# Performance work log

Measured on AMD Instinct MI355X. Metric: run time of the kernel, lower is better.

Reference implementation:

```python
import jax, jax.numpy as jnp
import numpy as np

B, S, EMB = 8, 1024, 512
H, DK = 8, 64
D_MODEL = 512


def setup_inputs() -> dict:
    key = jax.random.key(0)
    ks = jax.random.split(key, 12)
    s = 0.02
    return {
        "queries": jax.random.normal(ks[0], (B, S, EMB), jnp.float32),
        "keys": jax.random.normal(ks[1], (B, S, EMB), jnp.float32),
        "values": jax.random.normal(ks[2], (B, S, EMB), jnp.float32),
        "edges_key": jax.random.normal(ks[3], (S, S, DK), jnp.float32),
        "edges_value": jax.random.normal(ks[4], (S, S, DK), jnp.float32),
        "attn_bias": jax.random.normal(ks[5], (B, 1, S, S), jnp.float32),
        "Wq": jax.random.normal(ks[6], (EMB, H * DK), jnp.float32) * s,
        "bq": jnp.zeros((H * DK,), jnp.float32),
        "Wk": jax.random.normal(ks[7], (EMB, H * DK), jnp.float32) * s,
        "bk": jnp.zeros((H * DK,), jnp.float32),
        "Wv": jax.random.normal(ks[8], (EMB, H * DK), jnp.float32) * s,
        "bv": jnp.zeros((H * DK,), jnp.float32),
        "Wp": jax.random.normal(ks[9], (EMB, D_MODEL), jnp.float32) * s,
        "bp": jnp.zeros((D_MODEL,), jnp.float32),
    }


def _split_heads(x):
    b, s, _ = x.shape
    return x.reshape(b, s, H, DK).transpose(0, 2, 1, 3)  # [B,H,S,DK]


def reference(queries, keys, values, edges_key, edges_value, attn_bias,
              Wq, bq, Wk, bk, Wv, bv, Wp, bp):
    q = _split_heads(queries @ Wq + bq)
    k = _split_heads(keys @ Wk + bk)
    v = _split_heads(values @ Wv + bv)

    scaled_q = q * (DK ** -0.5)
    # standard scores + per-pair edge-key bias
    product = jnp.einsum('bhqd,bhkd->bhqk', scaled_q, k)
    edge_bias_k = jnp.einsum('bhqd,qkd->bhqk', scaled_q, edges_key)
    product = product + edge_bias_k + attn_bias

    weights = jax.nn.softmax(product, axis=-1)
    out = jnp.einsum('bhqk,bhkd->bhqd', weights, v)
    out = out + jnp.einsum('bhqk,qkd->bhqd', weights, edges_value)

    # combine heads: [B,H,S,DK] -> [B,S,H*DK]
    out = out.transpose(0, 2, 1, 3).reshape(queries.shape[0], queries.shape[1], H * DK)
    return out @ Wp + bp
```

## Files before the change

### kernel.cpp

```cpp
#include <hip/hip_runtime.h>
#include <cstdint>
#include <cstddef>


typedef __bf16 bf16x8 __attribute__((ext_vector_type(8)));
typedef float f32x4 __attribute__((ext_vector_type(4)));
typedef unsigned short u16x8 __attribute__((ext_vector_type(8)));
typedef unsigned short u16;

__device__ __forceinline__ u16 f2bf(float f) {
  unsigned int u = __float_as_uint(f);
  return (u16)((u + 0x7fffu + ((u >> 16) & 1u)) >> 16);
}

__device__ __forceinline__ float bf2f(u16 u) {
  return __uint_as_float(((unsigned int)u) << 16);
}

__device__ __forceinline__ bf16x8 ld8(const u16* p) {
  return __builtin_bit_cast(bf16x8, *(const u16x8*)p);
}

__device__ __forceinline__ bf16x8 cvt8(const float* p) {
  const float4 f1 = *(const float4*)p;
  const float4 f2 = *(const float4*)(p + 4);
  u16x8 u;
  u[0]=f2bf(f1.x); u[1]=f2bf(f1.y); u[2]=f2bf(f1.z); u[3]=f2bf(f1.w);
  u[4]=f2bf(f2.x); u[5]=f2bf(f2.y); u[6]=f2bf(f2.z); u[7]=f2bf(f2.w);
  return __builtin_bit_cast(bf16x8, u);
}

__device__ __forceinline__ f32x4 mfma16(bf16x8 a, bf16x8 b, f32x4 c) {
  return __builtin_amdgcn_mfma_f32_16x16x32_bf16(a, b, c, 0, 0, 0);
}

__global__ __launch_bounds__(256) void k0_weights(
    const float* __restrict__ Wq, const float* __restrict__ Wk,
    const float* __restrict__ Wv, const float* __restrict__ Wp,
    u16* __restrict__ WT) {
  const int idx = blockIdx.x * 256 + threadIdx.x;
  const int w = idx >> 18;
  const int rem = idx & 262143;
  const int o = rem >> 9, i = rem & 511;
  const float* W = (w == 0) ? Wq : (w == 1) ? Wk : (w == 2) ? Wv : Wp;
  WT[idx] = f2bf(W[(size_t)i * 512 + o]);
}

__global__ __launch_bounds__(256) void k0x(
    const float* __restrict__ Xq, const float* __restrict__ Xk,
    const float* __restrict__ Xv, u16* __restrict__ Xb) {
  const size_t idx = ((size_t)blockIdx.x * 256 + threadIdx.x) * 8;
  const int z = (int)(idx >> 22);
  const size_t rem = idx & 4194303u;
  const float* X = (z == 0) ? Xq : (z == 1) ? Xk : Xv;
  *(u16x8*)(Xb + idx) = __builtin_bit_cast(u16x8, cvt8(X + rem));
}

__global__ __launch_bounds__(256) void k1_proj(
    const u16* __restrict__ Xb, const float* __restrict__ bq,
    const float* __restrict__ bk, const float* __restrict__ bv,
    const u16* __restrict__ WT, u16* __restrict__ Qs, u16* __restrict__ Kb,
    u16* __restrict__ Vt) {
  const int z = blockIdx.z;
  const u16* X = Xb + (size_t)z * 4194304;
  const float* bias = (z == 0) ? bq : (z == 1) ? bk : bv;
  const u16* W = WT + (size_t)z * 512 * 512;
  const int mt = blockIdx.x, h = blockIdx.y;
  const int tid = threadIdx.x;
  const int wave = tid >> 6, lane = tid & 63;
  const int lm = lane & 15, quad = lane >> 4;
  const int row0 = mt * 64 + wave * 16;

  f32x4 acc0 = {0.f,0.f,0.f,0.f}, acc1 = {0.f,0.f,0.f,0.f};
  f32x4 acc2 = {0.f,0.f,0.f,0.f}, acc3 = {0.f,0.f,0.f,0.f};
  for (int kk = 0; kk < 512; kk += 32) {
    bf16x8 a = ld8(X + (size_t)(row0 + lm) * 512 + kk + quad * 8);
    acc0 = mfma16(a, ld8(W + (size_t)(h*64 +  0 + lm)*512 + kk + quad*8), acc0);
    acc1 = mfma16(a, ld8(W + (size_t)(h*64 + 16 + lm)*512 + kk + quad*8), acc1);
    acc2 = mfma16(a, ld8(W + (size_t)(h*64 + 32 + lm)*512 + kk + quad*8), acc2);
    acc3 = mfma16(a, ld8(W + (size_t)(h*64 + 48 + lm)*512 + kk + quad*8), acc3);
  }
  f32x4 acc[4] = {acc0, acc1, acc2, acc3};
#pragma unroll
  for (int n = 0; n < 4; n++) {
#pragma unroll
    for (int r = 0; r < 4; r++) {
      const int row = row0 + quad * 4 + r;
      const int b_ = row >> 10, s = row & 1023;
      const int d = n * 16 + lm;
      const float v = acc[n][r] + bias[h * 64 + d];
      const int bh = b_ * 8 + h;
      if (z == 0)      Qs[(((size_t)s) * 64 + bh) * 64 + d] = f2bf(v * 0.125f);
      else if (z == 1) Kb[(((size_t)bh) * 1024 + s) * 64 + d] = f2bf(v);
      else             Vt[(((size_t)bh) * 64 + d) * 1024 + s] = f2bf(v);
    }
  }
}

#define SC_QS 548
#define SC_BS 17
__global__ __launch_bounds__(256) void k2_scores(
    const u16* __restrict__ Qs, const u16* __restrict__ Kb,
    const float* __restrict__ EK, const float* __restrict__ BIAS,
    u16* __restrict__ P, float* __restrict__ Sc) {
  const int kb = blockIdx.x;
  const int qt = blockIdx.y;
  const int q0 = qt * 16;
  const int tid = threadIdx.x;
  const int wave = tid >> 6, lane = tid & 63;
  const int lm = lane & 15, quad = lane >> 4;

  __shared__ float scb[16 * SC_QS];

  float s_acc[2][2] = {{0.f, 0.f}, {0.f, 0.f}};

  for (int ks = 0; ks < 4; ks++) {
    const int kg = kb * 64 + ks * 16;
    for (int bhh = 0; bhh < 2; bhh++) {
      for (int t = 0; t < 8; t++) {
        const int bh = bhh * 32 + wave * 8 + t;
        const u16* aq = Qs + (((size_t)(q0 + lm)) * 64 + bh) * 64;
        const u16* bkp = Kb + ((size_t)bh * 1024 + (kg + lm)) * 64;
        f32x4 acc = {0.f,0.f,0.f,0.f};
        acc = mfma16(ld8(aq + quad * 8), ld8(bkp + quad * 8), acc);
        acc = mfma16(ld8(aq + 32 + quad * 8), ld8(bkp + 32 + quad * 8), acc);
        const int bhl = bh - bhh * 32;
#pragma unroll
        for (int r = 0; r < 4; r++)
          scb[(quad * 4 + r) * SC_QS + bhl * SC_BS + lm] = acc[r];
      }
      __syncthreads();
      for (int t = 0; t < 8; t++) {
        const int tileid = wave * 8 + t;
        const int q = tileid >> 1;
        const int bhl0 = (tileid & 1) * 16;
        const u16* aq =
            Qs + (((size_t)(q0 + q)) * 64 + bhh * 32 + bhl0 + lm) * 64;
        const float* be = EK + (((size_t)(q0 + q)) * 1024 + (kg + lm)) * 64;
        f32x4 acc = {0.f,0.f,0.f,0.f};
        acc = mfma16(ld8(aq + quad * 8), cvt8(be + quad * 8), acc);
        acc = mfma16(ld8(aq + 32 + quad * 8), cvt8(be + 32 + quad * 8), acc);
#pragma unroll
        for (int r = 0; r < 4; r++)
          scb[q * SC_QS + (bhl0 + quad * 4 + r) * SC_BS + lm] += acc[r];
      }
      __syncthreads();
      for (int rr = 0; rr < 2; rr++) {
        const int rl = rr * 256 + tid;
        const int q = rl >> 5, bhl = rl & 31;
        const int bh = bhh * 32 + bhl;
        const float* bp_ =
            BIAS + (((size_t)(bh >> 3)) * 1024 + q0 + q) * 1024 + kg;
        const float* scr = scb + q * SC_QS + bhl * SC_BS;
        float ss = 0.f;
        u16x8 o0, o1;
#pragma unroll
        for (int k = 0; k < 8; k++) {
          const float e = __expf(scr[k] + bp_[k]);
          ss += e; o0[k] = f2bf(e);
        }
#pragma unroll
        for (int k = 8; k < 16; k++) {
          const float e = __expf(scr[k] + bp_[k]);
          ss += e; o1[k - 8] = f2bf(e);
        }
        u16* pp = P + (((size_t)(q0 + q)) * 64 + bh) * 1024 + kg;
        *(u16x8*)pp = o0;
        *(u16x8*)(pp + 8) = o1;
        s_acc[bhh][rr] += ss;
      }
      __syncthreads();
    }
  }
#pragma unroll
  for (int bhh = 0; bhh < 2; bhh++) {
#pragma unroll
    for (int rr = 0; rr < 2; rr++) {
      const int rl = rr * 256 + tid;
      const int q = rl >> 5, bhl = rl & 31;
      const int bh = bhh * 32 + bhl;
      Sc[(((size_t)(q0 + q)) * 64 + bh) * 16 + kb] = s_acc[bhh][rr];
    }
  }
}

__global__ __launch_bounds__(256) void k2b_norm(
    const float* __restrict__ Sc, u16* __restrict__ P) {
  const int tid = threadIdx.x;
  const int wave = tid >> 6, lane = tid & 63;
  const size_t row = (size_t)blockIdx.x * 4 + wave;
  float s = Sc[row * 16 + (lane & 15)];
  s += __shfl_xor(s, 1);
  s += __shfl_xor(s, 2);
  s += __shfl_xor(s, 4);
  s += __shfl_xor(s, 8);
  const float corr = 1.f / s;
  u16* pp = P + row * 1024 + lane * 16;
  u16x8 v0 = *(u16x8*)pp;
  u16x8 v1 = *(u16x8*)(pp + 8);
#pragma unroll
  for (int j = 0; j < 8; j++) {
    v0[j] = f2bf(bf2f(v0[j]) * corr);
    v1[j] = f2bf(bf2f(v1[j]) * corr);
  }
  *(u16x8*)pp = v0;
  *(u16x8*)(pp + 8) = v1;
}

__global__ __launch_bounds__(256) void k3v(
    const u16* __restrict__ P, const u16* __restrict__ Vt,
    float* __restrict__ Of) {
  const int qt = blockIdx.x;
  const int bh = blockIdx.y;
  const int tid = threadIdx.x;
  const int wave = tid >> 6, lane = tid & 63;
  const int lm = lane & 15, quad = lane >> 4;
  const int m0 = qt * 64 + wave * 16;

  const u16* ap = P + (((size_t)(m0 + lm)) * 64 + bh) * 1024;
  const u16* vp = Vt + ((size_t)bh * 64) * 1024;
  f32x4 a0 = {0.f,0.f,0.f,0.f}, a1 = {0.f,0.f,0.f,0.f};
  f32x4 a2 = {0.f,0.f,0.f,0.f}, a3 = {0.f,0.f,0.f,0.f};
  for (int k = 0; k < 1024; k += 32) {
    const bf16x8 a = ld8(ap + k + quad * 8);
    a0 = mfma16(a, ld8(vp + ((size_t)( 0 + lm)) * 1024 + k + quad * 8), a0);
    a1 = mfma16(a, ld8(vp + ((size_t)(16 + lm)) * 1024 + k + quad * 8), a1);
    a2 = mfma16(a, ld8(vp + ((size_t)(32 + lm)) * 1024 + k + quad * 8), a2);
    a3 = mfma16(a, ld8(vp + ((size_t)(48 + lm)) * 1024 + k + quad * 8), a3);
  }
  f32x4 acc[4] = {a0, a1, a2, a3};
#pragma unroll
  for (int nt = 0; nt < 4; nt++) {
#pragma unroll
    for (int r = 0; r < 4; r++) {
      const int q = m0 + quad * 4 + r;
      const int d = nt * 16 + lm;
      Of[((size_t)q * 64 + bh) * 64 + d] = acc[nt][r];
    }
  }
}

__global__ __launch_bounds__(256) void k3e(
    const u16* __restrict__ P, const float* __restrict__ EV,
    const float* __restrict__ Of, u16* __restrict__ AO) {
  const int q = blockIdx.x;
  const int tid = threadIdx.x;
  const int wave = tid >> 6, lane = tid & 63;
  const int lm = lane & 15, quad = lane >> 4;

  __shared__ u16 evT[64 * 72];

  const float* evq = EV + (size_t)q * 65536;
  const u16* ap = P + (((size_t)q * 64) + wave * 16 + lm) * 1024;
  const int d4 = tid & 15, kx = tid >> 4;

  f32x4 a0 = {0.f,0.f,0.f,0.f}, a1 = {0.f,0.f,0.f,0.f};
  f32x4 a2 = {0.f,0.f,0.f,0.f}, a3 = {0.f,0.f,0.f,0.f};
  for (int slab = 0; slab < 16; slab++) {
    const int ks0 = slab * 64;
    __syncthreads();
#pragma unroll
    for (int it = 0; it < 4; it++) {
      const int k = it * 16 + kx;
      const float4 f = *(const float4*)(evq + (size_t)(ks0 + k) * 64 + d4 * 4);
      u16* w = evT + (d4 * 4) * 72 + k;
      w[0]   = f2bf(f.x);
      w[72]  = f2bf(f.y);
      w[144] = f2bf(f.z);
      w[216] = f2bf(f.w);
    }
    __syncthreads();
#pragma unroll
    for (int kk = 0; kk < 64; kk += 32) {
      const bf16x8 a = ld8(ap + ks0 + kk + quad * 8);
      a0 = mfma16(a, ld8(evT + ( 0 + lm) * 72 + kk + quad * 8), a0);
      a1 = mfma16(a, ld8(evT + (16 + lm) * 72 + kk + quad * 8), a1);
      a2 = mfma16(a, ld8(evT + (32 + lm) * 72 + kk + quad * 8), a2);
      a3 = mfma16(a, ld8(evT + (48 + lm) * 72 + kk + quad * 8), a3);
    }
  }
  f32x4 acc[4] = {a0, a1, a2, a3};
#pragma unroll
  for (int nt = 0; nt < 4; nt++) {
#pragma unroll
    for (int r = 0; r < 4; r++) {
      const int bh = wave * 16 + quad * 4 + r;
      const int d = nt * 16 + lm;
      const float o = Of[((size_t)q * 64 + bh) * 64 + d] + acc[nt][r];
      const int b = bh >> 3, h = bh & 7;
      AO[((size_t)(b * 1024 + q)) * 512 + h * 64 + d] = f2bf(o);
    }
  }
}

__global__ __launch_bounds__(256) void k4_proj(
    const u16* __restrict__ A, const u16* __restrict__ WpT,
    const float* __restrict__ bp, float* __restrict__ out) {
  const int mt = blockIdx.x, nt = blockIdx.y;
  const int tid = threadIdx.x;
  const int wave = tid >> 6, lane = tid & 63;
  const int lm = lane & 15, quad = lane >> 4;
  const int row0 = mt * 64 + wave * 16;
  f32x4 acc0 = {0.f,0.f,0.f,0.f}, acc1 = {0.f,0.f,0.f,0.f};
  f32x4 acc2 = {0.f,0.f,0.f,0.f}, acc3 = {0.f,0.f,0.f,0.f};
  for (int kk = 0; kk < 512; kk += 32) {
    bf16x8 a = ld8(A + (size_t)(row0 + lm) * 512 + kk + quad * 8);
    acc0 = mfma16(a, ld8(WpT + (size_t)(nt*64 +  0 + lm)*512 + kk + quad*8), acc0);
    acc1 = mfma16(a, ld8(WpT + (size_t)(nt*64 + 16 + lm)*512 + kk + quad*8), acc1);
    acc2 = mfma16(a, ld8(WpT + (size_t)(nt*64 + 32 + lm)*512 + kk + quad*8), acc2);
    acc3 = mfma16(a, ld8(WpT + (size_t)(nt*64 + 48 + lm)*512 + kk + quad*8), acc3);
  }
  f32x4 acc[4] = {acc0, acc1, acc2, acc3};
#pragma unroll
  for (int n = 0; n < 4; n++) {
#pragma unroll
    for (int r = 0; r < 4; r++) {
      const int row = row0 + quad * 4 + r;
      const int col = nt * 64 + n * 16 + lm;
      out[(size_t)row * 512 + col] = acc[n][r] + bp[col];
    }
  }
}

extern "C" void kernel_launch(void* const* d_in, const int* in_sizes, int n_in,
                              void* d_out, int out_size, void* d_ws,
                              size_t ws_size, hipStream_t stream) {
  const float* queries   = (const float*)d_in[0];
  const float* keys      = (const float*)d_in[1];
  const float* values    = (const float*)d_in[2];
  const float* edges_key = (const float*)d_in[3];
  const float* edges_val = (const float*)d_in[4];
  const float* attn_bias = (const float*)d_in[5];
  const float* Wq = (const float*)d_in[6];
  const float* bq = (const float*)d_in[7];
  const float* Wk = (const float*)d_in[8];
  const float* bk = (const float*)d_in[9];
  const float* Wv = (const float*)d_in[10];
  const float* bv = (const float*)d_in[11];
  const float* Wp = (const float*)d_in[12];
  const float* bp = (const float*)d_in[13];

  char* ws = (char*)d_ws;
  const size_t OFF_WT  = 0;
  const size_t OFF_QS  = OFF_WT  + (size_t)4*512*512*2;
  const size_t OFF_KB  = OFF_QS  + (size_t)1024*64*64*2;
  const size_t OFF_VT  = OFF_KB  + (size_t)1024*64*64*2;
  const size_t OFF_P   = OFF_VT  + (size_t)1024*64*64*2;
  const size_t OFF_SC  = OFF_P   + (size_t)1024*64*1024*2;

  u16*   WT  = (u16*)(ws + OFF_WT);
  u16*   Qs  = (u16*)(ws + OFF_QS);
  u16*   Kb  = (u16*)(ws + OFF_KB);
  u16*   Vt  = (u16*)(ws + OFF_VT);
  u16*   Pb  = (u16*)(ws + OFF_P);
  float* Sc  = (float*)(ws + OFF_SC);
  u16*   Xb  = (u16*)(ws + OFF_P);
  float* Of  = (float*)(ws + OFF_QS);
  u16*   AO  = (u16*)(ws + OFF_VT);

  k0_weights<<<4096, 256, 0, stream>>>(Wq, Wk, Wv, Wp, WT);
  k0x<<<6144, 256, 0, stream>>>(queries, keys, values, Xb);
  k1_proj<<<dim3(128, 8, 3), 256, 0, stream>>>(Xb, bq, bk, bv, WT, Qs, Kb, Vt);
  k2_scores<<<dim3(16, 64), 256, 0, stream>>>(Qs, Kb, edges_key, attn_bias,
                                              Pb, Sc);
  k2b_norm<<<16384, 256, 0, stream>>>(Sc, Pb);
  k3v<<<dim3(16, 64), 256, 0, stream>>>(Pb, Vt, Of);
  k3e<<<1024, 256, 0, stream>>>(Pb, edges_val, Of, AO);
  k4_proj<<<dim3(128, 8), 256, 0, stream>>>(AO, WT + (size_t)3*512*512, bp,
                                            (float*)d_out);
}
```

Baseline: 1.263 ms.

## Defer softmax normalization to PV epilogues, split score kernel over head halves, prefetch EV

Replaces the k2b_norm pass, which reread and rewrote the whole bf16 probability matrix, with a tiny kernel that computes per-row inverse sums. The 1/sum factor is now applied in the k3v and k3e epilogues. The score kernel is split across a grid z-dimension for the two head halves, which doubles the block count but makes each block reload the edge-key tile for its half. The k3e edge-value staging becomes double-buffered in shared memory with a register prefetch of the next slab. Launch-bounds occupancy hints are added, which may limit the register budget.

```diff
diff --git a/kernel.cpp b/kernel.cpp
--- a/kernel.cpp
+++ b/kernel.cpp
@@ -99,12 +99,13 @@
 
 #define SC_QS 548
 #define SC_BS 17
-__global__ __launch_bounds__(256) void k2_scores(
+__global__ __launch_bounds__(256, 4) void k2_scores(
     const u16* __restrict__ Qs, const u16* __restrict__ Kb,
     const float* __restrict__ EK, const float* __restrict__ BIAS,
     u16* __restrict__ P, float* __restrict__ Sc) {
   const int kb = blockIdx.x;
   const int qt = blockIdx.y;
+  const int bhh = blockIdx.z;
   const int q0 = qt * 16;
   const int tid = threadIdx.x;
   const int wave = tid >> 6, lane = tid & 63;
@@ -112,104 +113,87 @@
 
   __shared__ float scb[16 * SC_QS];
 
-  float s_acc[2][2] = {{0.f, 0.f}, {0.f, 0.f}};
+  float s_acc0 = 0.f, s_acc1 = 0.f;
 
   for (int ks = 0; ks < 4; ks++) {
     const int kg = kb * 64 + ks * 16;
-    for (int bhh = 0; bhh < 2; bhh++) {
-      for (int t = 0; t < 8; t++) {
-        const int bh = bhh * 32 + wave * 8 + t;
-        const u16* aq = Qs + (((size_t)(q0 + lm)) * 64 + bh) * 64;
-        const u16* bkp = Kb + ((size_t)bh * 1024 + (kg + lm)) * 64;
-        f32x4 acc = {0.f,0.f,0.f,0.f};
-        acc = mfma16(ld8(aq + quad * 8), ld8(bkp + quad * 8), acc);
-        acc = mfma16(ld8(aq + 32 + quad * 8), ld8(bkp + 32 + quad * 8), acc);
-        const int bhl = bh - bhh * 32;
-#pragma unroll
-        for (int r = 0; r < 4; r++)
-          scb[(quad * 4 + r) * SC_QS + bhl * SC_BS + lm] = acc[r];
-      }
-      __syncthreads();
-      for (int t = 0; t < 8; t++) {
-        const int tileid = wave * 8 + t;
-        const int q = tileid >> 1;
-        const int bhl0 = (tileid & 1) * 16;
-        const u16* aq =
-            Qs + (((size_t)(q0 + q)) * 64 + bhh * 32 + bhl0 + lm) * 64;
-        const float* be = EK + (((size_t)(q0 + q)) * 1024 + (kg + lm)) * 64;
-        f32x4 acc = {0.f,0.f,0.f,0.f};
-        acc = mfma16(ld8(aq + quad * 8), cvt8(be + quad * 8), acc);
-        acc = mfma16(ld8(aq + 32 + quad * 8), cvt8(be + 32 + quad * 8), acc);
-#pragma unroll
-        for (int r = 0; r < 4; r++)
-          scb[q * SC_QS + (bhl0 + quad * 4 + r) * SC_BS + lm] += acc[r];
-      }
-      __syncthreads();
-      for (int rr = 0; rr < 2; rr++) {
-        const int rl = rr * 256 + tid;
-        const int q = rl >> 5, bhl = rl & 31;
-        const int bh = bhh * 32 + bhl;
-        const float* bp_ =
-            BIAS + (((size_t)(bh >> 3)) * 1024 + q0 + q) * 1024 + kg;
-        const float* scr = scb + q * SC_QS + bhl * SC_BS;
-        float ss = 0.f;
-        u16x8 o0, o1;
-#pragma unroll
-        for (int k = 0; k < 8; k++) {
-          const float e = __expf(scr[k] + bp_[k]);
-          ss += e; o0[k] = f2bf(e);
-        }
-#pragma unroll
-        for (int k = 8; k < 16; k++) {
-          const float e = __expf(scr[k] + bp_[k]);
-          ss += e; o1[k - 8] = f2bf(e);
-        }
-        u16* pp = P + (((size_t)(q0 + q)) * 64 + bh) * 1024 + kg;
-        *(u16x8*)pp = o0;
-        *(u16x8*)(pp + 8) = o1;
-        s_acc[bhh][rr] += ss;
-      }
-      __syncthreads();
-    }
-  }
-#pragma unroll
-  for (int bhh = 0; bhh < 2; bhh++) {
+    for (int t = 0; t < 8; t++) {
+      const int bhl = wave * 8 + t;
+      const int bh = bhh * 32 + bhl;
+      const u16* aq = Qs + (((size_t)(q0 + lm)) * 64 + bh) * 64;
+      const u16* bkp = Kb + ((size_t)bh * 1024 + (kg + lm)) * 64;
+      f32x4 acc = {0.f,0.f,0.f,0.f};
+      acc = mfma16(ld8(aq + quad * 8), ld8(bkp + quad * 8), acc);
+      acc = mfma16(ld8(aq + 32 + quad * 8), ld8(bkp + 32 + quad * 8), acc);
+#pragma unroll
+      for (int r = 0; r < 4; r++)
+        scb[(quad * 4 + r) * SC_QS + bhl * SC_BS + lm] = acc[r];
+    }
+    __syncthreads();
+    for (int t = 0; t < 8; t++) {
+      const int tileid = wave * 8 + t;
+      const int q = tileid >> 1;
+      const int bhl0 = (tileid & 1) * 16;
+      const u16* aq =
+          Qs + (((size_t)(q0 + q)) * 64 + bhh * 32 + bhl0 + lm) * 64;
+      const float* be = EK + (((size_t)(q0 + q)) * 1024 + (kg + lm)) * 64;
+      f32x4 acc = {0.f,0.f,0.f,0.f};
+      acc = mfma16(ld8(aq + quad * 8), cvt8(be + quad * 8), acc);
+      acc = mfma16(ld8(aq + 32 + quad * 8), cvt8(be + 32 + quad * 8), acc);
+#pragma unroll
+      for (int r = 0; r < 4; r++)
+        scb[q * SC_QS + (bhl0 + quad * 4 + r) * SC_BS + lm] += acc[r];
+    }
+    __syncthreads();
 #pragma unroll
     for (int rr = 0; rr < 2; rr++) {
       const int rl = rr * 256 + tid;
       const int q = rl >> 5, bhl = rl & 31;
       const int bh = bhh * 32 + bhl;
-      Sc[(((size_t)(q0 + q)) * 64 + bh) * 16 + kb] = s_acc[bhh][rr];
-    }
-  }
-}
-
-__global__ __launch_bounds__(256) void k2b_norm(
-    const float* __restrict__ Sc, u16* __restrict__ P) {
-  const int tid = threadIdx.x;
-  const int wave = tid >> 6, lane = tid & 63;
-  const size_t row = (size_t)blockIdx.x * 4 + wave;
-  float s = Sc[row * 16 + (lane & 15)];
-  s += __shfl_xor(s, 1);
-  s += __shfl_xor(s, 2);
-  s += __shfl_xor(s, 4);
-  s += __shfl_xor(s, 8);
-  const float corr = 1.f / s;
-  u16* pp = P + row * 1024 + lane * 16;
-  u16x8 v0 = *(u16x8*)pp;
-  u16x8 v1 = *(u16x8*)(pp + 8);
-#pragma unroll
-  for (int j = 0; j < 8; j++) {
-    v0[j] = f2bf(bf2f(v0[j]) * corr);
-    v1[j] = f2bf(bf2f(v1[j]) * corr);
-  }
-  *(u16x8*)pp = v0;
-  *(u16x8*)(pp + 8) = v1;
+      const float* bp_ =
+          BIAS + (((size_t)(bh >> 3)) * 1024 + q0 + q) * 1024 + kg;
+      const float* scr = scb + q * SC_QS + bhl * SC_BS;
+      float ss = 0.f;
+      u16x8 o0, o1;
+#pragma unroll
+      for (int k = 0; k < 8; k++) {
+        const float e = __expf(scr[k] + bp_[k]);
+        ss += e; o0[k] = f2bf(e);
+      }
+#pragma unroll
+      for (int k = 8; k < 16; k++) {
+        const float e = __expf(scr[k] + bp_[k]);
+        ss += e; o1[k - 8] = f2bf(e);
+      }
+      u16* pp = P + (((size_t)(q0 + q)) * 64 + bh) * 1024 + kg;
+      *(u16x8*)pp = o0;
+      *(u16x8*)(pp + 8) = o1;
+      if (rr == 0) s_acc0 += ss; else s_acc1 += ss;
+    }
+    __syncthreads();
+  }
+#pragma unroll
+  for (int rr = 0; rr < 2; rr++) {
+    const int rl = rr * 256 + tid;
+    const int q = rl >> 5, bhl = rl & 31;
+    const int bh = bhh * 32 + bhl;
+    Sc[(((size_t)(q0 + q)) * 64 + bh) * 16 + kb] = (rr == 0) ? s_acc0 : s_acc1;
+  }
+}
+
+__global__ __launch_bounds__(256) void k2s_inv(
+    const float* __restrict__ Sc, float* __restrict__ Inv) {
+  const size_t row = (size_t)blockIdx.x * 256 + threadIdx.x;
+  const float4* p = (const float4*)(Sc + row * 16);
+  const float4 a = p[0], b = p[1], c = p[2], d = p[3];
+  const float s = ((a.x + a.y) + (a.z + a.w)) + ((b.x + b.y) + (b.z + b.w)) +
+                  ((c.x + c.y) + (c.z + c.w)) + ((d.x + d.y) + (d.z + d.w));
+  Inv[row] = 1.f / s;
 }
 
 __global__ __launch_bounds__(256) void k3v(
     const u16* __restrict__ P, const u16* __restrict__ Vt,
-    float* __restrict__ Of) {
+    const float* __restrict__ Inv, float* __restrict__ Of) {
   const int qt = blockIdx.x;
   const int bh = blockIdx.y;
   const int tid = threadIdx.x;
@@ -228,6 +212,10 @@
     a2 = mfma16(a, ld8(vp + ((size_t)(32 + lm)) * 1024 + k + quad * 8), a2);
     a3 = mfma16(a, ld8(vp + ((size_t)(48 + lm)) * 1024 + k + quad * 8), a3);
   }
+  float invr[4];
+#pragma unroll
+  for (int r = 0; r < 4; r++)
+    invr[r] = Inv[(size_t)(m0 + quad * 4 + r) * 64 + bh];
   f32x4 acc[4] = {a0, a1, a2, a3};
 #pragma unroll
   for (int nt = 0; nt < 4; nt++) {
@@ -235,50 +223,65 @@
     for (int r = 0; r < 4; r++) {
       const int q = m0 + quad * 4 + r;
       const int d = nt * 16 + lm;
-      Of[((size_t)q * 64 + bh) * 64 + d] = acc[nt][r];
-    }
-  }
-}
-
-__global__ __launch_bounds__(256) void k3e(
+      Of[((size_t)q * 64 + bh) * 64 + d] = acc[nt][r] * invr[r];
+    }
+  }
+}
+
+__global__ __launch_bounds__(256, 4) void k3e(
     const u16* __restrict__ P, const float* __restrict__ EV,
-    const float* __restrict__ Of, u16* __restrict__ AO) {
+    const float* __restrict__ Of, const float* __restrict__ Inv,
+    u16* __restrict__ AO) {
   const int q = blockIdx.x;
   const int tid = threadIdx.x;
   const int wave = tid >> 6, lane = tid & 63;
   const int lm = lane & 15, quad = lane >> 4;
 
-  __shared__ u16 evT[64 * 72];
+  __shared__ u16 evT[2][64 * 72];
 
   const float* evq = EV + (size_t)q * 65536;
   const u16* ap = P + (((size_t)q * 64) + wave * 16 + lm) * 1024;
   const int d4 = tid & 15, kx = tid >> 4;
 
+  float4 pf[4];
+#pragma unroll
+  for (int it = 0; it < 4; it++)
+    pf[it] = *(const float4*)(evq + (size_t)(it * 16 + kx) * 64 + d4 * 4);
+
   f32x4 a0 = {0.f,0.f,0.f,0.f}, a1 = {0.f,0.f,0.f,0.f};
   f32x4 a2 = {0.f,0.f,0.f,0.f}, a3 = {0.f,0.f,0.f,0.f};
   for (int slab = 0; slab < 16; slab++) {
+    const int buf = slab & 1;
     const int ks0 = slab * 64;
-    __syncthreads();
 #pragma unroll
     for (int it = 0; it < 4; it++) {
       const int k = it * 16 + kx;
-      const float4 f = *(const float4*)(evq + (size_t)(ks0 + k) * 64 + d4 * 4);
-      u16* w = evT + (d4 * 4) * 72 + k;
-      w[0]   = f2bf(f.x);
-      w[72]  = f2bf(f.y);
-      w[144] = f2bf(f.z);
-      w[216] = f2bf(f.w);
+      u16* w = evT[buf] + (d4 * 4) * 72 + k;
+      w[0]   = f2bf(pf[it].x);
+      w[72]  = f2bf(pf[it].y);
+      w[144] = f2bf(pf[it].z);
+      w[216] = f2bf(pf[it].w);
+    }
+    if (slab < 15) {
+#pragma unroll
+      for (int it = 0; it < 4; it++)
+        pf[it] = *(const float4*)(evq +
+                 (size_t)(ks0 + 64 + it * 16 + kx) * 64 + d4 * 4);
     }
     __syncthreads();
 #pragma unroll
     for (int kk = 0; kk < 64; kk += 32) {
       const bf16x8 a = ld8(ap + ks0 + kk + quad * 8);
-      a0 = mfma16(a, ld8(evT + ( 0 + lm) * 72 + kk + quad * 8), a0);
-      a1 = mfma16(a, ld8(evT + (16 + lm) * 72 + kk + quad * 8), a1);
-      a2 = mfma16(a, ld8(evT + (32 + lm) * 72 + kk + quad * 8), a2);
-      a3 = mfma16(a, ld8(evT + (48 + lm) * 72 + kk + quad * 8), a3);
-    }
-  }
+      a0 = mfma16(a, ld8(evT[buf] + ( 0 + lm) * 72 + kk + quad * 8), a0);
+      a1 = mfma16(a, ld8(evT[buf] + (16 + lm) * 72 + kk + quad * 8), a1);
+      a2 = mfma16(a, ld8(evT[buf] + (32 + lm) * 72 + kk + quad * 8), a2);
+      a3 = mfma16(a, ld8(evT[buf] + (48 + lm) * 72 + kk + quad * 8), a3);
+    }
+  }
+  float invr[4];
+#pragma unroll
+  for (int r = 0; r < 4; r++)
+    invr[r] = Inv[(size_t)q * 64 + wave * 16 + quad * 4 + r];
   f32x4 acc[4] = {a0, a1, a2, a3};
 #pragma unroll
   for (int nt = 0; nt < 4; nt++) {
@@ -286,7 +289,8 @@
     for (int r = 0; r < 4; r++) {
       const int bh = wave * 16 + quad * 4 + r;
       const int d = nt * 16 + lm;
-      const float o = Of[((size_t)q * 64 + bh) * 64 + d] + acc[nt][r];
+      const float o =
+          Of[((size_t)q * 64 + bh) * 64 + d] + acc[nt][r] * invr[r];
       const int b = bh >> 3, h = bh & 7;
       AO[((size_t)(b * 1024 + q)) * 512 + h * 64 + d] = f2bf(o);
     }
@@ -347,6 +351,7 @@
   const size_t OFF_VT  = OFF_KB  + (size_t)1024*64*64*2;
   const size_t OFF_P   = OFF_VT  + (size_t)1024*64*64*2;
   const size_t OFF_SC  = OFF_P   + (size_t)1024*64*1024*2;
+  const size_t OFF_INV = OFF_SC  + (size_t)65536*16*4;
 
   u16*   WT  = (u16*)(ws + OFF_WT);
   u16*   Qs  = (u16*)(ws + OFF_QS);
@@ -354,6 +359,7 @@
   u16*   Vt  = (u16*)(ws + OFF_VT);
   u16*   Pb  = (u16*)(ws + OFF_P);
   float* Sc  = (float*)(ws + OFF_SC);
+  float* Inv = (float*)(ws + OFF_INV);
   u16*   Xb  = (u16*)(ws + OFF_P);
   float* Of  = (float*)(ws + OFF_QS);
   u16*   AO  = (u16*)(ws + OFF_VT);
@@ -361,11 +367,11 @@
   k0_weights<<<4096, 256, 0, stream>>>(Wq, Wk, Wv, Wp, WT);
   k0x<<<6144, 256, 0, stream>>>(queries, keys, values, Xb);
   k1_proj<<<dim3(128, 8, 3), 256, 0, stream>>>(Xb, bq, bk, bv, WT, Qs, Kb, Vt);
-  k2_scores<<<dim3(16, 64), 256, 0, stream>>>(Qs, Kb, edges_key, attn_bias,
-                                              Pb, Sc);
-  k2b_norm<<<16384, 256, 0, stream>>>(Sc, Pb);
-  k3v<<<dim3(16, 64), 256, 0, stream>>>(Pb, Vt, Of);
-  k3e<<<1024, 256, 0, stream>>>(Pb, edges_val, Of, AO);
+  k2_scores<<<dim3(16, 64, 2), 256, 0, stream>>>(Qs, Kb, edges_key, attn_bias,
+                                                 Pb, Sc);
+  k2s_inv<<<256, 256, 0, stream>>>(Sc, Inv);
+  k3v<<<dim3(16, 64), 256, 0, stream>>>(Pb, Vt, Inv, Of);
+  k3e<<<1024, 256, 0, stream>>>(Pb, edges_val, Of, Inv, AO);
   k4_proj<<<dim3(128, 8), 256, 0, stream>>>(AO, WT + (size_t)3*512*512, bp,
                                             (float*)d_out);
 }
```

After: 1.193 ms. -5.5%, faster.
